# Kernel optimization log

Hardware: AMD Instinct MI355X
Metric: run time of the kernel (lower is better)

The kernel has to match this reference:

```python
import jax, jax.numpy as jnp
import numpy as np

B = 1_048_576
W = 64  # hidden width
N_FREQ = 6   # 3 dims * 6 freqs * (sin,cos) = 36
K_BLOB = 4   # one-blob bins per dim


def _freq_embed(p):
    # [B,3] -> [B,36]
    freqs = 2.0 ** jnp.arange(N_FREQ, dtype=p.dtype)
    ang = jnp.pi * p[:, :, None] * freqs  # [B,3,6]
    return jnp.concatenate([jnp.sin(ang), jnp.cos(ang)], axis=-1).reshape(p.shape[0], 3 * 2 * N_FREQ)


def _sph(d):
    # unit-square parameterization of a direction, [B,3] -> [B,2]
    d = d / (jnp.linalg.norm(d, axis=-1, keepdims=True) + 1e-8)
    u = jnp.arctan2(d[:, 1], d[:, 0]) / (2.0 * jnp.pi) + 0.5
    v = jnp.arccos(jnp.clip(d[:, 2], -1.0 + 1e-6, 1.0 - 1e-6)) / jnp.pi
    return jnp.stack([u, v], axis=-1)


def _one_blob(x, k=K_BLOB):
    # x in [0,1], [B,D] -> [B,D*k] Gaussian one-blob encoding
    centers = (jnp.arange(k, dtype=x.dtype) + 0.5) / k
    sigma = 1.0 / k
    g = jnp.exp(-0.5 * ((x[..., None] - centers) / sigma) ** 2)  # [B,D,k]
    return g.reshape(x.shape[0], -1)


def _encode(p, wi, n, alpha, beta, r):
    ones = jnp.ones((p.shape[0], 2), dtype=p.dtype)
    return jnp.concatenate([
        _freq_embed(p),                      # 36
        _one_blob(_sph(wi)),                 # 8
        _one_blob(_sph(n)),                  # 8
        _one_blob(1.0 - jnp.exp(-r)),        # 4
        alpha, beta,                         # 6
        ones,                                # 2 (implicit bias)
    ], axis=-1)                              # -> [B,64]


def _mlp(x, Ws):
    h = x
    for Wk in Ws[:-1]:
        h = jax.nn.relu(h @ Wk.T)
    return h @ Ws[-1].T  # [B,3]


def setup_inputs() -> dict:
    key = jax.random.key(0)
    ks = jax.random.split(key, 13)
    p = jax.random.normal(ks[0], (B, 3), jnp.float32)
    wi = jax.random.normal(ks[1], (B, 3), jnp.float32)
    n = jax.random.normal(ks[2], (B, 3), jnp.float32)
    alpha = jax.random.uniform(ks[3], (B, 3), jnp.float32)
    beta = jax.random.uniform(ks[4], (B, 3), jnp.float32)
    r = jax.random.uniform(ks[5], (B, 1), jnp.float32)
    s = 1.0 / np.sqrt(W)
    weights = {}
    for i in range(6):
        weights[f"W{i}"] = jax.random.normal(ks[6 + i], (W, W), jnp.float32) * s
    weights["W6"] = jax.random.normal(ks[12], (3, W), jnp.float32) * s
    return dict(p=p, wi=wi, n=n, alpha=alpha, beta=beta, r=r, **weights)


def reference(p, wi, n, alpha, beta, r, W0, W1, W2, W3, W4, W5, W6):
    x = _encode(p, wi, n, alpha, beta, r)
    out = _mlp(x, [W0, W1, W2, W3, W4, W5, W6])
    return out * (alpha + beta)  # reflectance factorization
```

## Files before the change

kernel.cpp:

```cpp
#include <hip/hip_runtime.h>


typedef _Float16 f16;
typedef f16 f16x2 __attribute__((ext_vector_type(2)));
typedef f16 f16x4 __attribute__((ext_vector_type(4)));
typedef f16 f16x8 __attribute__((ext_vector_type(8)));
typedef float f32x4 __attribute__((ext_vector_type(4)));

#define MFMA32(A, B, C) __builtin_amdgcn_mfma_f32_16x16x32_f16(A, B, C, 0, 0, 0)
#define LDS_FENCE() __asm__ volatile("" ::: "memory")

static constexpr int TILES = 4;
static constexpr int WAVES = 8;
static constexpr int BLOCK = WAVES * 64;
static constexpr int SPB   = WAVES * 64;

static constexpr int    WUNITS   = 50;
static constexpr int    WCHUNKS  = WUNITS * 64;
static constexpr size_t WS_BYTES = (size_t)WCHUNKS * 16;
static constexpr int    LDS_W    = 51200;

__host__ __device__ __forceinline__ int tau(int x) {
    return (x & 32) + ((x & 7) >> 2) * 16 + ((x >> 3) & 3) * 4 + (x & 3);
}

__device__ __forceinline__ f16x2 pkh(float a, float b) {
    return __builtin_bit_cast(f16x2, __builtin_amdgcn_cvt_pkrtz(a, b));
}

__device__ __forceinline__ f16x8 pack8(const float* f) {
    f16x2 a = pkh(f[0], f[1]);
    f16x2 b = pkh(f[2], f[3]);
    f16x2 c = pkh(f[4], f[5]);
    f16x2 d = pkh(f[6], f[7]);
    f16x8 v;
    v[0] = a[0]; v[1] = a[1]; v[2] = b[0]; v[3] = b[1];
    v[4] = c[0]; v[5] = c[1]; v[6] = d[0]; v[7] = d[1];
    return v;
}

__device__ __forceinline__ f16x4 pack4(f32x4 v) {
    f16x2 a = pkh(v[0], v[1]);
    f16x2 b = pkh(v[2], v[3]);
    f16x4 r;
    r[0] = a[0]; r[1] = a[1]; r[2] = b[0]; r[3] = b[1];
    return r;
}

__device__ __forceinline__ float fast_atan2_rev(float y, float x) {
    const float ax = __builtin_fabsf(x), ay = __builtin_fabsf(y);
    const float mx = fmaxf(ax, ay), mn = fminf(ax, ay);
    const float a = mn * __builtin_amdgcn_rcpf(fmaxf(mx, 1e-30f));
    const float s = a * a;
    float r = a * (0.99997726f + s * (-0.33262347f + s * (0.19354346f +
              s * (-0.11643287f + s * (0.05265332f - s * 0.01172120f)))));
    if (ay > ax) r = 1.5707963268f - r;
    if (x < 0.0f) r = 3.1415926536f - r;
    r = (y < 0.0f) ? -r : r;
    return r * 0.15915494309189535f;
}

__device__ __forceinline__ float fast_acos(float x) {
    const float ax = __builtin_fabsf(x);
    const float t = __builtin_amdgcn_sqrtf(1.0f - ax);
    const float p = t * (1.5707288f + ax * (-0.2121144f +
                    ax * (0.0742610f - ax * 0.0187293f)));
    return (x < 0.0f) ? (3.1415926536f - p) : p;
}

__device__ __forceinline__ void blob4(float x, float* out) {
    const float dx = x - 0.125f;
    const float E0 = __expf(-8.0f * dx * dx);
    const float R  = __expf(4.0f * dx);
    const float t1 = R * 0.60653066f;
    const float t2 = R * 0.22313016f;
    const float t3 = R * 0.082084999f;
    out[0] = E0;
    out[1] = E0 * t1;
    out[2] = out[1] * t2;
    out[3] = out[2] * t3;
}

__device__ __forceinline__ f16x8 make_wchunk(
    int c, const float* __restrict__ W0, const float* __restrict__ W1,
    const float* __restrict__ W2, const float* __restrict__ W3,
    const float* __restrict__ W4, const float* __restrict__ W5,
    const float* __restrict__ W6)
{
    const int lane2 = c & 63;
    const int unit  = c >> 6;
    const int q = lane2 >> 4, m = lane2 & 15;
    f16x8 v;
    if (unit < 48) {
        const int l = unit >> 3, kt = (unit & 7) >> 2, mt = unit & 3;
        const float* Ws[6] = {W0, W1, W2, W3, W4, W5};
        const float* __restrict__ Wl = Ws[l];
#pragma unroll
        for (int j = 0; j < 8; ++j) {
            const int x = kt * 32 + q * 8 + j;
            const int src = (l == 0) ? x : tau(x);
            v[j] = (f16)Wl[(mt * 16 + m) * 64 + src];
        }
    } else {
        const int kt = unit - 48;
#pragma unroll
        for (int j = 0; j < 8; ++j) {
            const int src = tau(kt * 32 + q * 8 + j);
            v[j] = (m < 3) ? (f16)W6[m * 64 + src] : (f16)0.0f;
        }
    }
    return v;
}

__global__ __launch_bounds__(256, 1) void pack_weights_kernel(
    const float* __restrict__ W0, const float* __restrict__ W1,
    const float* __restrict__ W2, const float* __restrict__ W3,
    const float* __restrict__ W4, const float* __restrict__ W5,
    const float* __restrict__ W6, f16* __restrict__ ws)
{
    const int c = (int)blockIdx.x * 256 + threadIdx.x;
    if (c >= WCHUNKS) return;
    *(f16x8*)(ws + (size_t)c * 8) = make_wchunk(c, W0, W1, W2, W3, W4, W5, W6);
}

__device__ __forceinline__ f16x8 cat44(f16x4 a, f16x4 b) {
    return __builtin_shufflevector(a, b, 0, 1, 2, 3, 4, 5, 6, 7);
}

template<int PACKED>
__global__ __launch_bounds__(BLOCK, 4) void nrc_mlp_kernel(
    const float* __restrict__ P,  const float* __restrict__ WI,
    const float* __restrict__ NV, const float* __restrict__ AL,
    const float* __restrict__ BE, const float* __restrict__ RR,
    const f16*   __restrict__ ws,
    const float* __restrict__ W0, const float* __restrict__ W1,
    const float* __restrict__ W2, const float* __restrict__ W3,
    const float* __restrict__ W4, const float* __restrict__ W5,
    const float* __restrict__ W6, float* __restrict__ Out)
{
    __shared__ __attribute__((aligned(16))) unsigned char smem[LDS_W];

    const int tid  = threadIdx.x;
    const int lane = tid & 63;
    const int w    = tid >> 6;
    const int q    = lane >> 4;
    const int m    = lane & 15;
    unsigned char* const hb = smem + w * 2048;

    const int wave_base = (int)blockIdx.x * SPB + w * 64;

    float feat[64];
    float ab0, ab1, ab2;

    {
        const int s = wave_base + lane;

        float pv[3], wv[3], nv[3], av[3], bv[3];
#pragma unroll
        for (int d = 0; d < 3; ++d) {
            pv[d] = P [s * 3 + d];
            wv[d] = WI[s * 3 + d];
            nv[d] = NV[s * 3 + d];
            av[d] = AL[s * 3 + d];
            bv[d] = BE[s * 3 + d];
        }
        const float rv = RR[s];

#pragma unroll
        for (int d = 0; d < 3; ++d) {
            const float fr = __builtin_amdgcn_fractf(pv[d] * 0.5f);
            float sv = __builtin_amdgcn_sinf(fr);
            float cv = __builtin_amdgcn_cosf(fr);
            feat[d * 12 + 0] = sv;
            feat[d * 12 + 6] = cv;
#pragma unroll
            for (int k = 1; k < 6; ++k) {
                const float s2 = sv * sv;
                const float sc = sv * cv;
                cv = fmaf(-2.0f, s2, 1.0f);
                sv = sc + sc;
                feat[d * 12 + k]     = sv;
                feat[d * 12 + 6 + k] = cv;
            }
        }
#pragma unroll
        for (int which = 0; which < 2; ++which) {
            const float* dv = (which == 0) ? wv : nv;
            const int fo = 36 + which * 8;
            const float nr = __builtin_amdgcn_sqrtf(dv[0]*dv[0] + dv[1]*dv[1] + dv[2]*dv[2]) + 1e-8f;
            const float u  = fast_atan2_rev(dv[1], dv[0]) + 0.5f;
            float zc = dv[2] * __builtin_amdgcn_rcpf(nr);
            zc = fminf(fmaxf(zc, -1.0f + 1e-6f), 1.0f - 1e-6f);
            const float vv = fast_acos(zc) * 0.3183098861837907f;
            blob4(u,  &feat[fo]);
            blob4(vv, &feat[fo + 4]);
        }
        blob4(1.0f - __expf(-rv), &feat[52]);

        feat[56] = av[0]; feat[57] = av[1]; feat[58] = av[2];
        feat[59] = bv[0]; feat[60] = bv[1]; feat[61] = bv[2];
        feat[62] = 1.0f;  feat[63] = 1.0f;

        ab0 = av[0] + bv[0];
        ab1 = av[1] + bv[1];
        ab2 = av[2] + bv[2];
    }

    const int te = lane >> 4;
    f16x8 bf[TILES][2];
#pragma unroll
    for (int pass = 0; pass < TILES; ++pass) {
        if (te == pass) {
            unsigned char* const tb = hb + m * 128;
#pragma unroll
            for (int g = 0; g < 8; ++g) {
                const int slot0 = (4 * g + 4 * m) & 31;
                *(f16x8*)(tb + slot0 * 4) = pack8(&feat[g * 8]);
            }
        }
        LDS_FENCE();
#pragma unroll
        for (int kt = 0; kt < 2; ++kt) {
            const int s0 = (16 * kt + 4 * q + 4 * m) & 31;
            bf[pass][kt] = *(const f16x8*)(hb + m * 128 + s0 * 4);
        }
        LDS_FENCE();
    }

    __syncthreads();

#pragma unroll
    for (int i = 0; i < (WCHUNKS + BLOCK - 1) / BLOCK; ++i) {
        const int c = i * BLOCK + tid;
        if (c < WCHUNKS) {
            f16x8 v;
            if (PACKED) v = *(const f16x8*)(ws + (size_t)c * 8);
            else        v = make_wchunk(c, W0, W1, W2, W3, W4, W5, W6);
            *(f16x8*)(smem + c * 16) = v;
        }
    }
    __syncthreads();

    const f16x4 zero4 = {(f16)0.0f, (f16)0.0f, (f16)0.0f, (f16)0.0f};
    unsigned char* const wb = smem + lane * 16;

#pragma unroll
    for (int layer = 0; layer < 6; ++layer) {
        f16x8 wa[8];
#pragma unroll
        for (int f = 0; f < 8; ++f)
            wa[f] = *(const f16x8*)(wb + (layer * 8 + f) * 1024);

#pragma unroll
        for (int t = 0; t < TILES; ++t) {
            f32x4 acc[4];
#pragma unroll
            for (int mt = 0; mt < 4; ++mt) {
                f32x4 z = {0.0f, 0.0f, 0.0f, 0.0f};
                z = MFMA32(wa[mt],     bf[t][0], z);
                z = MFMA32(wa[4 + mt], bf[t][1], z);
                acc[mt] = z;
            }
            f16x4 pk[4];
#pragma unroll
            for (int mt = 0; mt < 4; ++mt)
                pk[mt] = __builtin_elementwise_max(pack4(acc[mt]), zero4);
            bf[t][0] = cat44(pk[0], pk[1]);
            bf[t][1] = cat44(pk[2], pk[3]);
        }
    }

    {
        const f16x8 w6f0 = *(const f16x8*)(wb + 48 * 1024);
        const f16x8 w6f1 = *(const f16x8*)(wb + 49 * 1024);
#pragma unroll
        for (int t = 0; t < TILES; ++t) {
            f32x4 z = {0.0f, 0.0f, 0.0f, 0.0f};
            z = MFMA32(w6f0, bf[t][0], z);
            z = MFMA32(w6f1, bf[t][1], z);
            const int src = t * 16 + m;
            const float s0 = __shfl(ab0, src);
            const float s1 = __shfl(ab1, src);
            const float s2 = __shfl(ab2, src);
            if (lane < 16) {
                const int s = wave_base + t * 16 + m;
                float* o = Out + s * 3;
                o[0] = z[0] * s0;
                o[1] = z[1] * s1;
                o[2] = z[2] * s2;
            }
        }
    }
}

extern "C" void kernel_launch(void* const* d_in, const int* in_sizes, int n_in,
                              void* d_out, int out_size, void* d_ws, size_t ws_size,
                              hipStream_t stream) {
    (void)n_in; (void)out_size;
    const float* P  = (const float*)d_in[0];
    const float* WI = (const float*)d_in[1];
    const float* NV = (const float*)d_in[2];
    const float* AL = (const float*)d_in[3];
    const float* BE = (const float*)d_in[4];
    const float* RR = (const float*)d_in[5];
    const float* W0 = (const float*)d_in[6];
    const float* W1 = (const float*)d_in[7];
    const float* W2 = (const float*)d_in[8];
    const float* W3 = (const float*)d_in[9];
    const float* W4 = (const float*)d_in[10];
    const float* W5 = (const float*)d_in[11];
    const float* W6 = (const float*)d_in[12];
    f16*   ws  = (f16*)d_ws;
    float* Out = (float*)d_out;

    const int Bn = in_sizes[0] / 3;
    const int grid = Bn / SPB;

    if (ws_size >= WS_BYTES) {
        hipLaunchKernelGGL(pack_weights_kernel, dim3((WCHUNKS + 255) / 256),
                           dim3(256), 0, stream, W0, W1, W2, W3, W4, W5, W6, ws);
        hipLaunchKernelGGL((nrc_mlp_kernel<1>), dim3(grid), dim3(BLOCK), 0, stream,
                           P, WI, NV, AL, BE, RR, ws,
                           W0, W1, W2, W3, W4, W5, W6, Out);
    } else {
        hipLaunchKernelGGL((nrc_mlp_kernel<0>), dim3(grid), dim3(BLOCK), 0, stream,
                           P, WI, NV, AL, BE, RR, ws,
                           W0, W1, W2, W3, W4, W5, W6, Out);
    }
}
```

Before: 154.0 us.

## Stream hidden weights to LDS asynchronously and keep output layer in registers

Hidden-layer weight staging now uses global_load_lds direct-to-LDS copies instead of loading through registers and storing. The final-layer weights are loaded straight into registers at kernel start, which shrinks LDS from 50 KB to 48 KB. The launch bound goes from 4 to 6 blocks per SM for more occupancy. The aim is to cut weight-staging latency and register pressure per block, at the risk of register spills under the tighter launch bound.

```diff
diff --git a/kernel.cpp b/kernel.cpp
--- a/kernel.cpp
+++ b/kernel.cpp
@@ -18,7 +18,9 @@
 static constexpr int    WUNITS   = 50;
 static constexpr int    WCHUNKS  = WUNITS * 64;
 static constexpr size_t WS_BYTES = (size_t)WCHUNKS * 16;
-static constexpr int    LDS_W    = 51200;
+static constexpr int    HUNITS   = 48;
+static constexpr int    HCHUNKS  = HUNITS * 64;
+static constexpr int    LDS_W    = HUNITS * 1024;
 
 __host__ __device__ __forceinline__ int tau(int x) {
     return (x & 32) + ((x & 7) >> 2) * 16 + ((x >> 3) & 3) * 4 + (x & 3);
@@ -127,8 +129,15 @@
     return __builtin_shufflevector(a, b, 0, 1, 2, 3, 4, 5, 6, 7);
 }
 
+__device__ __forceinline__ void async_ld16(const void* g, void* l) {
+    __builtin_amdgcn_global_load_lds(
+        (const __attribute__((address_space(1))) void*)g,
+        (__attribute__((address_space(3))) void*)l,
+        16, 0, 0);
+}
+
 template<int PACKED>
-__global__ __launch_bounds__(BLOCK, 4) void nrc_mlp_kernel(
+__global__ __launch_bounds__(BLOCK, 6) void nrc_mlp_kernel(
     const float* __restrict__ P,  const float* __restrict__ WI,
     const float* __restrict__ NV, const float* __restrict__ AL,
     const float* __restrict__ BE, const float* __restrict__ RR,
@@ -149,6 +158,15 @@
 
     const int wave_base = (int)blockIdx.x * SPB + w * 64;
 
+    f16x8 w6f0, w6f1;
+    if (PACKED) {
+        w6f0 = *(const f16x8*)(ws + (size_t)(HCHUNKS + lane) * 8);
+        w6f1 = *(const f16x8*)(ws + (size_t)(HCHUNKS + 64 + lane) * 8);
+    } else {
+        w6f0 = make_wchunk(HCHUNKS + lane,      W0, W1, W2, W3, W4, W5, W6);
+        w6f1 = make_wchunk(HCHUNKS + 64 + lane, W0, W1, W2, W3, W4, W5, W6);
+    }
+
     float feat[64];
     float ab0, ab1, ab2;
 
@@ -229,19 +247,23 @@
 
     __syncthreads();
 
-#pragma unroll
-    for (int i = 0; i < (WCHUNKS + BLOCK - 1) / BLOCK; ++i) {
-        const int c = i * BLOCK + tid;
-        if (c < WCHUNKS) {
-            f16x8 v;
-            if (PACKED) v = *(const f16x8*)(ws + (size_t)c * 8);
-            else        v = make_wchunk(c, W0, W1, W2, W3, W4, W5, W6);
-            *(f16x8*)(smem + c * 16) = v;
+    if (PACKED) {
+#pragma unroll
+        for (int i = 0; i < HCHUNKS / BLOCK; ++i) {
+            const int c = i * BLOCK + tid;
+            async_ld16(ws + (size_t)c * 8, smem + c * 16);
+        }
+    } else {
+#pragma unroll
+        for (int i = 0; i < HCHUNKS / BLOCK; ++i) {
+            const int c = i * BLOCK + tid;
+            *(f16x8*)(smem + c * 16) = make_wchunk(c, W0, W1, W2, W3, W4, W5, W6);
         }
     }
     __syncthreads();
 
     const f16x4 zero4 = {(f16)0.0f, (f16)0.0f, (f16)0.0f, (f16)0.0f};
+    const f32x4 ZF = {0.0f, 0.0f, 0.0f, 0.0f};
     unsigned char* const wb = smem + lane * 16;
 
 #pragma unroll
@@ -256,8 +278,7 @@
             f32x4 acc[4];
 #pragma unroll
             for (int mt = 0; mt < 4; ++mt) {
-                f32x4 z = {0.0f, 0.0f, 0.0f, 0.0f};
-                z = MFMA32(wa[mt],     bf[t][0], z);
+                f32x4 z = MFMA32(wa[mt], bf[t][0], ZF);
                 z = MFMA32(wa[4 + mt], bf[t][1], z);
                 acc[mt] = z;
             }
@@ -271,12 +292,9 @@
     }
 
     {
-        const f16x8 w6f0 = *(const f16x8*)(wb + 48 * 1024);
-        const f16x8 w6f1 = *(const f16x8*)(wb + 49 * 1024);
 #pragma unroll
         for (int t = 0; t < TILES; ++t) {
-            f32x4 z = {0.0f, 0.0f, 0.0f, 0.0f};
-            z = MFMA32(w6f0, bf[t][0], z);
+            f32x4 z = MFMA32(w6f0, bf[t][0], ZF);
             z = MFMA32(w6f1, bf[t][1], z);
             const int src = t * 16 + m;
             const float s0 = __shfl(ab0, src);
```

Measured after the change: 303.3 us. +96.9%, slower.
